# Kernel optimization log

Measured on AMD Instinct MI355X. Metric: run time of the kernel, lower is better.

## Reference

```python
import jax, jax.numpy as jnp
import numpy as np

HEAD_SIZE = 128  # embeddings_dims // no_of_heads = 4096 // 32


def apply_rope(v):
    # v: [B, S, d] with d = HEAD_SIZE; interleaved-pair rotation as in source
    B, S, d = v.shape
    pos = jnp.arange(S, dtype=jnp.float32)[:, None]              # [S, 1]
    idx = jnp.arange(0, d, 2, dtype=jnp.float32)[None, :]        # [1, d//2]
    theta = jnp.power(10000.0, -2.0 * idx / d)                   # [1, d//2]
    angles = pos * theta                                         # [S, d//2]
    cos = jnp.cos(angles)
    sin = jnp.sin(angles)
    vr = v.reshape(B, S, d // 2, 2)
    x0, x1 = vr[..., 0], vr[..., 1]
    out = jnp.stack([x0 * cos - x1 * sin, x1 * cos + x0 * sin], axis=-1)
    return out.reshape(B, S, d)


def setup_inputs() -> dict:
    key = jax.random.key(0)
    kx, kq, kk, kv = jax.random.split(key, 4)
    B, S, D = 2, 4096, 4096
    d = HEAD_SIZE
    scale = 1.0 / np.sqrt(D)
    return {
        "x": jax.random.normal(kx, (B, S, D), dtype=jnp.float32),
        "Wq": jax.random.normal(kq, (d, D), dtype=jnp.float32) * scale,
        "Wk": jax.random.normal(kk, (d, D), dtype=jnp.float32) * scale,
        "Wv": jax.random.normal(kv, (d, D), dtype=jnp.float32) * scale,
    }


def reference(x, Wq, Wk, Wv):
    # single attention head, non-flash path (eval mode: dropout = identity)
    B, S, D = x.shape
    q = jnp.einsum('bsd,hd->bsh', x, Wq)  # [B, S, head]
    k = jnp.einsum('bsd,hd->bsh', x, Wk)
    v = jnp.einsum('bsd,hd->bsh', x, Wv)
    q = apply_rope(q)
    k = apply_rope(k)
    scale = k.shape[-1] ** (-0.5)
    scores = jnp.einsum('bqh,bkh->bqk', q, k) * scale  # [B, S, S]
    causal = jnp.tril(jnp.ones((S, S), dtype=bool))
    scores = jnp.where(causal, scores, -jnp.inf)
    weights = jax.nn.softmax(scores, axis=-1)
    out = jnp.einsum('bqk,bkh->bqh', weights, v)  # [B, S, head]
    return out
```

## Files before the change

### kernel.cpp

```cpp
#include <hip/hip_runtime.h>

typedef _Float16 half8 __attribute__((ext_vector_type(8)));
typedef float f32x4 __attribute__((ext_vector_type(4)));

#define S_LEN 4096
#define D_DIM 4096
#define HD 128


#define ASTR 40
#define BSTR 40
#define QSTR 136
#define VSTR 72
__global__ __launch_bounds__(256) void proj_kernel(const float* __restrict__ x,
                                                   const float* __restrict__ wq,
                                                   const float* __restrict__ wk,
                                                   const float* __restrict__ wv,
                                                   _Float16* __restrict__ qw,
                                                   _Float16* __restrict__ kw,
                                                   _Float16* __restrict__ vt) {
    __shared__ __align__(16) _Float16 smem[128 * VSTR];
    _Float16* Ash = smem;
    _Float16* Bsh = smem + 64 * ASTR;
    const int tid = threadIdx.x;
    const int bx = blockIdx.x;
    const int M0 = blockIdx.y * 64;
    const float* w = (bx == 0) ? wq : (bx == 1) ? wk : wv;
    const int lane = tid & 63, wv_ = tid >> 6;
    const int l15 = lane & 15, quad = lane >> 4;

    const int arow = tid >> 2, acol = (tid & 3) * 8;
    const int brow = tid >> 1, bcol = (tid & 1) * 16;
    const float* xa = x + (size_t)(M0 + arow) * D_DIM + acol;
    const float* wb = w + (size_t)brow * D_DIM + bcol;
    _Float16* ash = &Ash[arow * ASTR + acol];
    _Float16* bsh = &Bsh[brow * BSTR + bcol];

    f32x4 acc[8];
    for (int ni = 0; ni < 8; ++ni) acc[ni] = (f32x4){0.f, 0.f, 0.f, 0.f};

    float4 a0 = *(const float4*)(xa);
    float4 a1 = *(const float4*)(xa + 4);
    float4 b0 = *(const float4*)(wb);
    float4 b1 = *(const float4*)(wb + 4);
    float4 b2 = *(const float4*)(wb + 8);
    float4 b3 = *(const float4*)(wb + 12);

    for (int k0 = 0; k0 < D_DIM; k0 += 32) {
        half8 ha = { (_Float16)a0.x, (_Float16)a0.y, (_Float16)a0.z, (_Float16)a0.w,
                     (_Float16)a1.x, (_Float16)a1.y, (_Float16)a1.z, (_Float16)a1.w };
        half8 hb0 = { (_Float16)b0.x, (_Float16)b0.y, (_Float16)b0.z, (_Float16)b0.w,
                      (_Float16)b1.x, (_Float16)b1.y, (_Float16)b1.z, (_Float16)b1.w };
        half8 hb1 = { (_Float16)b2.x, (_Float16)b2.y, (_Float16)b2.z, (_Float16)b2.w,
                      (_Float16)b3.x, (_Float16)b3.y, (_Float16)b3.z, (_Float16)b3.w };
        *(half8*)ash = ha;
        *(half8*)bsh = hb0;
        *(half8*)(bsh + 8) = hb1;
        __syncthreads();
        if (k0 + 32 < D_DIM) {
            a0 = *(const float4*)(xa + k0 + 32);
            a1 = *(const float4*)(xa + k0 + 36);
            b0 = *(const float4*)(wb + k0 + 32);
            b1 = *(const float4*)(wb + k0 + 36);
            b2 = *(const float4*)(wb + k0 + 40);
            b3 = *(const float4*)(wb + k0 + 44);
        }
        half8 af = *(const half8*)&Ash[(wv_ * 16 + l15) * ASTR + quad * 8];
        half8 bf[8];
        for (int ni = 0; ni < 8; ++ni)
            bf[ni] = *(const half8*)&Bsh[(ni * 16 + l15) * BSTR + quad * 8];
        for (int ni = 0; ni < 8; ++ni)
            acc[ni] = __builtin_amdgcn_mfma_f32_16x16x32_f16(af, bf[ni], acc[ni], 0, 0, 0);
        __syncthreads();
    }

    if (bx < 2) {
        for (int ni = 0; ni < 8; ++ni) {
            const int hd = ni * 16 + l15;
            const float theta = exp2f((float)(hd >> 1) * -0.4152410118609203f);
            for (int r = 0; r < 4; ++r) {
                const int row = wv_ * 16 + quad * 4 + r;
                const int s = (M0 + row) & (S_LEN - 1);
                float v = acc[ni][r];
                float sn, cn;
                sincosf((float)s * theta, &sn, &cn);
                float vp = __shfl_xor(v, 1);
                v = (l15 & 1) ? fmaf(v, cn, vp * sn) : fmaf(v, cn, -vp * sn);
                smem[row * QSTR + hd] = (_Float16)v;
            }
        }
        __syncthreads();
        _Float16* dst = ((bx == 0) ? qw : kw) + (size_t)M0 * HD;
        const int row = tid >> 2, c0 = (tid & 3) * 32;
        for (int j = 0; j < 4; ++j) {
            half8 v = *(const half8*)&smem[row * QSTR + c0 + j * 8];
            *(half8*)&dst[row * HD + c0 + j * 8] = v;
        }
    } else {
        for (int ni = 0; ni < 8; ++ni) {
            const int hd = ni * 16 + l15;
            for (int r = 0; r < 4; ++r) {
                const int row = wv_ * 16 + quad * 4 + r;
                smem[hd * VSTR + row] = (_Float16)acc[ni][r];
            }
        }
        __syncthreads();
        _Float16* dst = vt + ((size_t)(M0 >> 12) * HD) * S_LEN + (M0 & (S_LEN - 1));
        const int hd = tid >> 1, s0 = (tid & 1) * 32;
        for (int j = 0; j < 4; ++j) {
            half8 v = *(const half8*)&smem[hd * VSTR + s0 + j * 8];
            *(half8*)&dst[(size_t)hd * S_LEN + s0 + j * 8] = v;
        }
    }
}

template<bool MASKED>
__device__ __forceinline__ void attn_tile(int kbase, int qg, int l15, int quad,
                                          const _Float16* __restrict__ kb,
                                          const _Float16* __restrict__ vtb,
                                          const half8* bq, f32x4* acc,
                                          float& mrun, float& lrun) {
    const float csc = 0.1275174348796053f;
    const _Float16* kr = kb + (size_t)(kbase + l15) * HD + quad * 8;
    f32x4 st0 = (f32x4){0.f, 0.f, 0.f, 0.f};
    f32x4 st1 = (f32x4){0.f, 0.f, 0.f, 0.f};
    for (int kk = 0; kk < 4; ++kk) {
        half8 k0 = *(const half8*)(kr + kk * 32);
        half8 k1 = *(const half8*)(kr + 16 * HD + kk * 32);
        st0 = __builtin_amdgcn_mfma_f32_16x16x32_f16(k0, bq[kk], st0, 0, 0, 0);
        st1 = __builtin_amdgcn_mfma_f32_16x16x32_f16(k1, bq[kk], st1, 0, 0, 0);
    }
    half8 va[8];
    const _Float16* vr = vtb + (size_t)l15 * S_LEN + kbase + quad * 8;
    for (int c = 0; c < 8; ++c)
        va[c] = *(const half8*)(vr + (size_t)c * 16 * S_LEN);
    float p0[4], p1[4];
    float mloc = -1e30f;
    for (int r = 0; r < 4; ++r) {
        float v0 = st0[r] * csc;
        float v1 = st1[r] * csc;
        if (MASKED) {
            const int key0 = kbase + quad * 4 + r;
            if (key0 > qg)      v0 = -1e30f;
            if (key0 + 16 > qg) v1 = -1e30f;
        }
        p0[r] = v0; p1[r] = v1;
        mloc = fmaxf(mloc, fmaxf(v0, v1));
    }
    mloc = fmaxf(mloc, __shfl_xor(mloc, 16));
    mloc = fmaxf(mloc, __shfl_xor(mloc, 32));
    const float mnew = fmaxf(mrun, mloc);
    const float alpha = exp2f(mrun - mnew);
    mrun = mnew;
    float ls = 0.f;
    for (int r = 0; r < 4; ++r) {
        p0[r] = exp2f(p0[r] - mnew);
        p1[r] = exp2f(p1[r] - mnew);
        ls += p0[r] + p1[r];
    }
    ls += __shfl_xor(ls, 16);
    ls += __shfl_xor(ls, 32);
    lrun = lrun * alpha + ls;
    for (int c = 0; c < 8; ++c)
        acc[c] *= alpha;
    int ph0 = __builtin_bit_cast(int, __builtin_amdgcn_cvt_pkrtz(p0[0], p0[1]));
    int ph1 = __builtin_bit_cast(int, __builtin_amdgcn_cvt_pkrtz(p0[2], p0[3]));
    int ph2 = __builtin_bit_cast(int, __builtin_amdgcn_cvt_pkrtz(p1[0], p1[1]));
    int ph3 = __builtin_bit_cast(int, __builtin_amdgcn_cvt_pkrtz(p1[2], p1[3]));
    const int s0 = (l15 + (((quad << 1)    ) & 3) * 16) * 4;
    const int s1 = (l15 + (((quad << 1) + 1) & 3) * 16) * 4;
    int a0 = __builtin_amdgcn_ds_bpermute(s0, ph0);
    int a1 = __builtin_amdgcn_ds_bpermute(s0, ph1);
    int a2 = __builtin_amdgcn_ds_bpermute(s1, ph0);
    int a3 = __builtin_amdgcn_ds_bpermute(s1, ph1);
    int b0 = __builtin_amdgcn_ds_bpermute(s0, ph2);
    int b1 = __builtin_amdgcn_ds_bpermute(s0, ph3);
    int b2 = __builtin_amdgcn_ds_bpermute(s1, ph2);
    int b3 = __builtin_amdgcn_ds_bpermute(s1, ph3);
    const bool lo = quad < 2;
    int4 pi = { lo ? a0 : b0, lo ? a1 : b1, lo ? a2 : b2, lo ? a3 : b3 };
    half8 pf = __builtin_bit_cast(half8, pi);
    for (int c = 0; c < 8; ++c)
        acc[c] = __builtin_amdgcn_mfma_f32_16x16x32_f16(va[c], pf, acc[c], 0, 0, 0);
}

__global__ __launch_bounds__(256) void attn_kernel(const _Float16* __restrict__ q,
                                                   const _Float16* __restrict__ k,
                                                   const _Float16* __restrict__ vt,
                                                   float* __restrict__ out) {
    __shared__ __align__(16) float Osh[4][16][132];
    __shared__ float msh[4][16];
    __shared__ float lsh[4][16];
    const int tid = threadIdx.x;
    const int lane = tid & 63, wv_ = tid >> 6;
    const int l15 = lane & 15, quad = lane >> 4;
    const int bidx = blockIdx.x;
    const int b = bidx & 1;
    const int t = 255 - (bidx >> 1);
    const int qb = t * 16;
    const int qg = qb + l15;

    const _Float16* qp = q + (size_t)(b * S_LEN + qb) * HD;
    half8 bq[4];
    for (int kk = 0; kk < 4; ++kk)
        bq[kk] = *(const half8*)&qp[l15 * HD + kk * 32 + quad * 8];

    f32x4 acc[8];
    for (int c = 0; c < 8; ++c) acc[c] = (f32x4){0.f, 0.f, 0.f, 0.f};
    float mrun = -1e30f, lrun = 0.f;

    const _Float16* kb = k + (size_t)b * S_LEN * HD;
    const _Float16* vtb = vt + (size_t)b * HD * S_LEN;

    const int nfull = (qb + 1) >> 5;
    for (int kt = wv_; kt < nfull; kt += 4)
        attn_tile<false>(kt * 32, qg, l15, quad, kb, vtb, bq, acc, mrun, lrun);
    if ((nfull & 3) == wv_)
        attn_tile<true>(nfull * 32, qg, l15, quad, kb, vtb, bq, acc, mrun, lrun);

    for (int c = 0; c < 8; ++c)
        *(f32x4*)&Osh[wv_][l15][c * 16 + quad * 4] = acc[c];
    if (quad == 0) { msh[wv_][l15] = mrun; lsh[wv_][l15] = lrun; }
    __syncthreads();

    const int qr = tid >> 4, dg = (tid & 15) * 8;
    float m0 = msh[0][qr], m1 = msh[1][qr], m2 = msh[2][qr], m3 = msh[3][qr];
    float mm = fmaxf(fmaxf(m0, m1), fmaxf(m2, m3));
    float f0 = exp2f(m0 - mm), f1 = exp2f(m1 - mm), f2 = exp2f(m2 - mm), f3 = exp2f(m3 - mm);
    float l = lsh[0][qr] * f0 + lsh[1][qr] * f1 + lsh[2][qr] * f2 + lsh[3][qr] * f3;
    f32x4 oa = (f32x4){0.f, 0.f, 0.f, 0.f}, ob = oa;
    oa += *(f32x4*)&Osh[0][qr][dg] * f0;  ob += *(f32x4*)&Osh[0][qr][dg + 4] * f0;
    oa += *(f32x4*)&Osh[1][qr][dg] * f1;  ob += *(f32x4*)&Osh[1][qr][dg + 4] * f1;
    oa += *(f32x4*)&Osh[2][qr][dg] * f2;  ob += *(f32x4*)&Osh[2][qr][dg + 4] * f2;
    oa += *(f32x4*)&Osh[3][qr][dg] * f3;  ob += *(f32x4*)&Osh[3][qr][dg + 4] * f3;
    const float inv = 1.0f / l;
    float* op = out + (size_t)(b * S_LEN + qb + qr) * HD + dg;
    *(float4*)op       = (float4){oa[0] * inv, oa[1] * inv, oa[2] * inv, oa[3] * inv};
    *(float4*)(op + 4) = (float4){ob[0] * inv, ob[1] * inv, ob[2] * inv, ob[3] * inv};
}

extern "C" void kernel_launch(void* const* d_in, const int* in_sizes, int n_in,
                              void* d_out, int out_size, void* d_ws, size_t ws_size,
                              hipStream_t stream) {
    const float* x  = (const float*)d_in[0];
    const float* Wq = (const float*)d_in[1];
    const float* Wk = (const float*)d_in[2];
    const float* Wv = (const float*)d_in[3];
    float* out = (float*)d_out;
    char* ws = (char*)d_ws;
    _Float16* qw = (_Float16*)(ws);
    _Float16* kw = (_Float16*)(ws + (2u << 20));
    _Float16* vt = (_Float16*)(ws + (4u << 20));

    proj_kernel<<<dim3(3, 128), dim3(256), 0, stream>>>(x, Wq, Wk, Wv, qw, kw, vt);
    attn_kernel<<<dim3(512), dim3(256), 0, stream>>>(qw, kw, vt, out);
}
```

Baseline: 374.0 us.

## Enlarge projection tile to 128 rows with 2x2 wave grid, move RoPE to separate kernel

The projection kernel now computes a 128x128 output tile per block, with each wave owning a 64x64 sub-tile of 4x4 MFMA fragments. This raises arithmetic intensity per LDS load and halves how often each weight tile is reloaded per row. RoPE is taken out of the projection epilogue and runs as a separate elementwise kernel over the fp16 Q and K buffers. The trade-offs are fewer blocks (192, fewer than the CU count), more registers per wave, and an extra launch with another pass over Q/K.

```diff
diff --git a/kernel.cpp b/kernel.cpp
--- a/kernel.cpp
+++ b/kernel.cpp
@@ -1,6 +1,7 @@
 #include <hip/hip_runtime.h>
 
 typedef _Float16 half8 __attribute__((ext_vector_type(8)));
+typedef _Float16 half2v __attribute__((ext_vector_type(2)));
 typedef float f32x4 __attribute__((ext_vector_type(4)));
 
 #define S_LEN 4096
@@ -9,9 +10,7 @@
 
 
 #define ASTR 40
-#define BSTR 40
 #define QSTR 136
-#define VSTR 72
 __global__ __launch_bounds__(256) void proj_kernel(const float* __restrict__ x,
                                                    const float* __restrict__ wq,
                                                    const float* __restrict__ wk,
@@ -19,99 +18,115 @@
                                                    _Float16* __restrict__ qw,
                                                    _Float16* __restrict__ kw,
                                                    _Float16* __restrict__ vt) {
-    __shared__ __align__(16) _Float16 smem[128 * VSTR];
+    __shared__ __align__(16) _Float16 smem[128 * QSTR];
     _Float16* Ash = smem;
-    _Float16* Bsh = smem + 64 * ASTR;
+    _Float16* Bsh = smem + 128 * ASTR;
     const int tid = threadIdx.x;
     const int bx = blockIdx.x;
-    const int M0 = blockIdx.y * 64;
+    const int M0 = blockIdx.y * 128;
     const float* w = (bx == 0) ? wq : (bx == 1) ? wk : wv;
-    const int lane = tid & 63, wv_ = tid >> 6;
+    const int lane = tid & 63, wid = tid >> 6;
+    const int wr = wid >> 1, wc = wid & 1;
     const int l15 = lane & 15, quad = lane >> 4;
 
-    const int arow = tid >> 2, acol = (tid & 3) * 8;
-    const int brow = tid >> 1, bcol = (tid & 1) * 16;
-    const float* xa = x + (size_t)(M0 + arow) * D_DIM + acol;
-    const float* wb = w + (size_t)brow * D_DIM + bcol;
-    _Float16* ash = &Ash[arow * ASTR + acol];
-    _Float16* bsh = &Bsh[brow * BSTR + bcol];
-
-    f32x4 acc[8];
-    for (int ni = 0; ni < 8; ++ni) acc[ni] = (f32x4){0.f, 0.f, 0.f, 0.f};
+    const int srow = tid >> 1, scol = (tid & 1) * 16;
+    const float* xa = x + (size_t)(M0 + srow) * D_DIM + scol;
+    const float* wb = w + (size_t)srow * D_DIM + scol;
+    _Float16* ash = &Ash[srow * ASTR + scol];
+    _Float16* bsh = &Bsh[srow * ASTR + scol];
+
+    f32x4 acc[4][4];
+    for (int mi = 0; mi < 4; ++mi)
+        for (int ni = 0; ni < 4; ++ni)
+            acc[mi][ni] = (f32x4){0.f, 0.f, 0.f, 0.f};
 
     float4 a0 = *(const float4*)(xa);
     float4 a1 = *(const float4*)(xa + 4);
+    float4 a2 = *(const float4*)(xa + 8);
+    float4 a3 = *(const float4*)(xa + 12);
     float4 b0 = *(const float4*)(wb);
     float4 b1 = *(const float4*)(wb + 4);
     float4 b2 = *(const float4*)(wb + 8);
     float4 b3 = *(const float4*)(wb + 12);
 
     for (int k0 = 0; k0 < D_DIM; k0 += 32) {
-        half8 ha = { (_Float16)a0.x, (_Float16)a0.y, (_Float16)a0.z, (_Float16)a0.w,
-                     (_Float16)a1.x, (_Float16)a1.y, (_Float16)a1.z, (_Float16)a1.w };
+        half8 ha0 = { (_Float16)a0.x, (_Float16)a0.y, (_Float16)a0.z, (_Float16)a0.w,
+                      (_Float16)a1.x, (_Float16)a1.y, (_Float16)a1.z, (_Float16)a1.w };
+        half8 ha1 = { (_Float16)a2.x, (_Float16)a2.y, (_Float16)a2.z, (_Float16)a2.w,
+                      (_Float16)a3.x, (_Float16)a3.y, (_Float16)a3.z, (_Float16)a3.w };
         half8 hb0 = { (_Float16)b0.x, (_Float16)b0.y, (_Float16)b0.z, (_Float16)b0.w,
                       (_Float16)b1.x, (_Float16)b1.y, (_Float16)b1.z, (_Float16)b1.w };
         half8 hb1 = { (_Float16)b2.x, (_Float16)b2.y, (_Float16)b2.z, (_Float16)b2.w,
                       (_Float16)b3.x, (_Float16)b3.y, (_Float16)b3.z, (_Float16)b3.w };
-        *(half8*)ash = ha;
+        *(half8*)ash = ha0;
+        *(half8*)(ash + 8) = ha1;
         *(half8*)bsh = hb0;
         *(half8*)(bsh + 8) = hb1;
         __syncthreads();
         if (k0 + 32 < D_DIM) {
             a0 = *(const float4*)(xa + k0 + 32);
             a1 = *(const float4*)(xa + k0 + 36);
+            a2 = *(const float4*)(xa + k0 + 40);
+            a3 = *(const float4*)(xa + k0 + 44);
             b0 = *(const float4*)(wb + k0 + 32);
             b1 = *(const float4*)(wb + k0 + 36);
             b2 = *(const float4*)(wb + k0 + 40);
             b3 = *(const float4*)(wb + k0 + 44);
         }
-        half8 af = *(const half8*)&Ash[(wv_ * 16 + l15) * ASTR + quad * 8];
-        half8 bf[8];
-        for (int ni = 0; ni < 8; ++ni)
-            bf[ni] = *(const half8*)&Bsh[(ni * 16 + l15) * BSTR + quad * 8];
-        for (int ni = 0; ni < 8; ++ni)
-            acc[ni] = __builtin_amdgcn_mfma_f32_16x16x32_f16(af, bf[ni], acc[ni], 0, 0, 0);
+        half8 af[4], bf[4];
+        for (int mi = 0; mi < 4; ++mi)
+            af[mi] = *(const half8*)&Ash[(wr * 64 + mi * 16 + l15) * ASTR + quad * 8];
+        for (int ni = 0; ni < 4; ++ni)
+            bf[ni] = *(const half8*)&Bsh[(wc * 64 + ni * 16 + l15) * ASTR + quad * 8];
+        for (int mi = 0; mi < 4; ++mi)
+            for (int ni = 0; ni < 4; ++ni)
+                acc[mi][ni] = __builtin_amdgcn_mfma_f32_16x16x32_f16(af[mi], bf[ni],
+                                                                     acc[mi][ni], 0, 0, 0);
         __syncthreads();
     }
 
     if (bx < 2) {
-        for (int ni = 0; ni < 8; ++ni) {
-            const int hd = ni * 16 + l15;
-            const float theta = exp2f((float)(hd >> 1) * -0.4152410118609203f);
-            for (int r = 0; r < 4; ++r) {
-                const int row = wv_ * 16 + quad * 4 + r;
-                const int s = (M0 + row) & (S_LEN - 1);
-                float v = acc[ni][r];
-                float sn, cn;
-                sincosf((float)s * theta, &sn, &cn);
-                float vp = __shfl_xor(v, 1);
-                v = (l15 & 1) ? fmaf(v, cn, vp * sn) : fmaf(v, cn, -vp * sn);
-                smem[row * QSTR + hd] = (_Float16)v;
-            }
-        }
+        for (int mi = 0; mi < 4; ++mi)
+            for (int ni = 0; ni < 4; ++ni)
+                for (int r = 0; r < 4; ++r)
+                    smem[(wr * 64 + mi * 16 + quad * 4 + r) * QSTR +
+                         wc * 64 + ni * 16 + l15] = (_Float16)acc[mi][ni][r];
         __syncthreads();
         _Float16* dst = ((bx == 0) ? qw : kw) + (size_t)M0 * HD;
-        const int row = tid >> 2, c0 = (tid & 3) * 32;
-        for (int j = 0; j < 4; ++j) {
-            half8 v = *(const half8*)&smem[row * QSTR + c0 + j * 8];
-            *(half8*)&dst[row * HD + c0 + j * 8] = v;
-        }
+        const int row = tid >> 1, c0 = (tid & 1) * 64;
+        for (int j = 0; j < 8; ++j)
+            *(half8*)&dst[row * HD + c0 + j * 8] = *(const half8*)&smem[row * QSTR + c0 + j * 8];
     } else {
-        for (int ni = 0; ni < 8; ++ni) {
-            const int hd = ni * 16 + l15;
-            for (int r = 0; r < 4; ++r) {
-                const int row = wv_ * 16 + quad * 4 + r;
-                smem[hd * VSTR + row] = (_Float16)acc[ni][r];
-            }
-        }
-        __syncthreads();
-        _Float16* dst = vt + ((size_t)(M0 >> 12) * HD) * S_LEN + (M0 & (S_LEN - 1));
-        const int hd = tid >> 1, s0 = (tid & 1) * 32;
-        for (int j = 0; j < 4; ++j) {
-            half8 v = *(const half8*)&smem[hd * VSTR + s0 + j * 8];
-            *(half8*)&dst[(size_t)hd * S_LEN + s0 + j * 8] = v;
-        }
-    }
+        for (int mi = 0; mi < 4; ++mi)
+            for (int ni = 0; ni < 4; ++ni)
+                for (int r = 0; r < 4; ++r)
+                    smem[(wc * 64 + ni * 16 + l15) * QSTR +
+                         wr * 64 + mi * 16 + quad * 4 + r] = (_Float16)acc[mi][ni][r];
+        __syncthreads();
+        _Float16* dst = vt + (size_t)(M0 >> 12) * HD * S_LEN + (M0 & (S_LEN - 1));
+        const int hd = tid >> 1, c0 = (tid & 1) * 64;
+        for (int j = 0; j < 8; ++j)
+            *(half8*)&dst[(size_t)hd * S_LEN + c0 + j * 8] =
+                *(const half8*)&smem[hd * QSTR + c0 + j * 8];
+    }
+}
+
+__global__ __launch_bounds__(256) void rope_kernel(_Float16* __restrict__ qw,
+                                                   _Float16* __restrict__ kw) {
+    const int g = blockIdx.x * 256 + threadIdx.x;
+    const int m = g >> 6, p = g & 63;
+    const int s = m & (S_LEN - 1);
+    const float theta = exp2f((float)p * -0.4152410118609203f);
+    float sn, cn;
+    sincosf((float)s * theta, &sn, &cn);
+    const size_t off = (size_t)m * HD + 2 * p;
+    half2v qv = *(half2v*)&qw[off];
+    half2v kv = *(half2v*)&kw[off];
+    float q0 = qv[0], q1 = qv[1], k0 = kv[0], k1 = kv[1];
+    half2v qo = { (_Float16)(q0 * cn - q1 * sn), (_Float16)(q1 * cn + q0 * sn) };
+    half2v ko = { (_Float16)(k0 * cn - k1 * sn), (_Float16)(k1 * cn + k0 * sn) };
+    *(half2v*)&qw[off] = qo;
+    *(half2v*)&kw[off] = ko;
 }
 
 template<bool MASKED>
@@ -252,6 +267,7 @@
     _Float16* kw = (_Float16*)(ws + (2u << 20));
     _Float16* vt = (_Float16*)(ws + (4u << 20));
 
-    proj_kernel<<<dim3(3, 128), dim3(256), 0, stream>>>(x, Wq, Wk, Wv, qw, kw, vt);
+    proj_kernel<<<dim3(3, 64), dim3(256), 0, stream>>>(x, Wq, Wk, Wv, qw, kw, vt);
+    rope_kernel<<<dim3(2048), dim3(256), 0, stream>>>(qw, kw);
     attn_kernel<<<dim3(512), dim3(256), 0, stream>>>(qw, kw, vt, out);
 }
```

New measurement: 399.3 us. +6.8%, slower.
